# Kernel tuning notes

Hardware: AMD Instinct MI355X
Metric: run time of the kernel (lower is better)

The kernel has to match this reference:

```python
import jax, jax.numpy as jnp
import numpy as np
import math

B, S, D, H, WIDTH, NHW = 8, 1024, 512, 8, 8, 2
DK = D // H
S2 = S + 2 * WIDTH


def setup_inputs() -> dict:
    key = jax.random.key(0)
    ks = jax.random.split(key, 12)
    sc = 1.0 / math.sqrt(D)
    return {
        "x": jax.random.normal(ks[0], (B, S, D), jnp.float32),
        "l_attn_W": jax.random.normal(ks[1], (4, D, D), jnp.float32) * sc,  # q,k,v,out
        "l_attn_b": jnp.zeros((4, D), jnp.float32),
        "r_attn_W": jax.random.normal(ks[2], (4, D, D), jnp.float32) * sc,
        "r_attn_b": jnp.zeros((4, D), jnp.float32),
        "left_pad": jax.random.normal(ks[3], (WIDTH, D), jnp.float32) * sc,
        "right_pad": jax.random.normal(ks[4], (WIDTH, D), jnp.float32) * sc,
        "left_w": jax.random.normal(ks[5], (WIDTH + 1,), jnp.float32),
        "right_w": jax.random.normal(ks[6], (WIDTH + 1,), jnp.float32),
        "l_hw_W": jax.random.normal(ks[7], (NHW, D, 2 * D), jnp.float32) * sc,
        "l_hw_b": jnp.zeros((NHW, 2 * D), jnp.float32),
        "r_hw_W": jax.random.normal(ks[8], (NHW, D, 2 * D), jnp.float32) * sc,
        "r_hw_b": jnp.zeros((NHW, 2 * D), jnp.float32),
    }


def _mha(x, W, b, mask):
    # x: [B, S2, D]; W: [4, D, D]; mask: [1, S2, S2] bool (True = keep)
    q = (x @ W[0] + b[0]).reshape(B, S2, H, DK)
    k = (x @ W[1] + b[1]).reshape(B, S2, H, DK)
    v = (x @ W[2] + b[2]).reshape(B, S2, H, DK)
    scores = jnp.einsum('bihd,bjhd->bhij', q, k) / math.sqrt(DK)
    scores = jnp.where(mask[:, None], scores, jnp.float32(-1e9))
    p = jax.nn.softmax(scores, axis=-1)
    o = jnp.einsum('bhij,bjhd->bihd', p, v).reshape(B, S2, D)
    return o @ W[3] + b[3]


def _highway(x, Ws, bs):
    # AllenNLP-style Highway: projected -> [nonlinear | gate]
    for i in range(NHW):
        proj = x @ Ws[i] + bs[i]
        nl = jax.nn.relu(proj[..., :D])
        g = jax.nn.sigmoid(proj[..., D:])
        x = g * x + (1.0 - g) * nl
    return x


def reference(x, l_attn_W, l_attn_b, r_attn_W, r_attn_b, left_pad, right_pad,
              left_w, right_w, l_hw_W, l_hw_b, r_hw_W, r_hw_b):
    new_in = jnp.concatenate([
        jnp.broadcast_to(left_pad, (B, WIDTH, D)), x,
        jnp.broadcast_to(right_pad, (B, WIDTH, D))], axis=1)  # [B, S2, D]
    idx = jnp.arange(S2)
    diff = idx[:, None] - idx[None, :]
    lmask = ((diff >= 0) & (diff <= WIDTH + 1))[None]          # attend to [i-width-1, i]
    rmask = ((diff <= 0) & (diff >= -(WIDTH + 1)))[None]       # attend to [i, i+width+1]
    nl_attn = _mha(new_in, l_attn_W, l_attn_b, lmask)
    nr_attn = _mha(new_in, r_attn_W, r_attn_b, rmask)
    left_out = nl_attn[:, WIDTH:WIDTH + S, :]   # position end = start + width
    right_out = nr_attn[:, WIDTH:WIDTH + S, :]
    # relative-position weighted sliding windows (vectorized over all steps)
    lrel = sum(left_w[j] * new_in[:, j:j + S, :] for j in range(WIDTH + 1))
    rrel = sum(right_w[j] * new_in[:, WIDTH + j:WIDTH + j + S, :] for j in range(WIDTH + 1))
    left_out = _highway(left_out + lrel, l_hw_W, l_hw_b)
    right_out = _highway(right_out + rrel, r_hw_W, r_hw_b)
    out = jnp.concatenate([left_out, right_out], axis=-1)  # [B, S, 2D]
    return out[None]  # [1, B, S, 2D] matching torch stack layout
```

## Files before the change

### kernel.cpp

```cpp
#include <hip/hip_runtime.h>


#define B_ 8
#define S_ 1024
#define D_ 512
#define H_ 8
#define DK_ 64
#define WIDTH_ 8
#define S2_ 1040
#define NHW_ 2

typedef short bf16x8 __attribute__((ext_vector_type(8)));
typedef float f32x4 __attribute__((ext_vector_type(4)));

__device__ __forceinline__ float us2f(unsigned short u) {
  union { unsigned int i; float f; } c; c.i = ((unsigned int)u) << 16; return c.f;
}
__device__ __forceinline__ unsigned short f2us(float f) {
  union { float f; unsigned int i; } c; c.f = f;
  unsigned int x = c.i;
  return (unsigned short)((x + 0x7fffu + ((x >> 16) & 1u)) >> 16);
}
__device__ __forceinline__ unsigned int pack2(float a, float b) {
  return (unsigned int)f2us(a) | ((unsigned int)f2us(b) << 16);
}
__device__ __forceinline__ void async16(const void* g, void* l) {
  __builtin_amdgcn_global_load_lds(
      (const __attribute__((address_space(1))) void*)g,
      (__attribute__((address_space(3))) void*)l, 16, 0, 0);
}
__device__ __forceinline__ void unpack8(uint4 u, float* f) {
  unsigned int w[4] = {u.x, u.y, u.z, u.w};
  #pragma unroll
  for (int c = 0; c < 4; ++c) {
    union { unsigned int i; float g; } lo, hi;
    lo.i = w[c] << 16;
    hi.i = w[c] & 0xffff0000u;
    f[2 * c] = lo.g;
    f[2 * c + 1] = hi.g;
  }
}

__global__ __launch_bounds__(256) void k_transpose_attn(
    const float* __restrict__ lW, const float* __restrict__ rW,
    unsigned short* __restrict__ WTall, unsigned short* __restrict__ WTp)
{
  __shared__ float tile[32][33];
  const size_t DD = (size_t)D_ * D_;
  int z = blockIdx.z, side = z >> 2, slice = z & 3;
  const float* src = (side ? rW : lW) + (size_t)slice * DD;
  unsigned short* dst = (slice < 3) ? WTall + ((size_t)(side * 3 + slice)) * DD
                                    : WTp + (size_t)side * DD;
  int c0 = blockIdx.x * 32, r0 = blockIdx.y * 32;
  int tx = threadIdx.x & 31, ty = threadIdx.x >> 5;
  #pragma unroll
  for (int i = 0; i < 4; ++i)
    tile[ty + i * 8][tx] = src[(size_t)(r0 + ty + i * 8) * D_ + c0 + tx];
  __syncthreads();
  #pragma unroll
  for (int i = 0; i < 4; ++i)
    dst[(size_t)(c0 + ty + i * 8) * D_ + r0 + tx] = f2us(tile[tx][ty + i * 8]);
}

__global__ __launch_bounds__(256) void k_transpose_hw(
    const float* __restrict__ lhwW, const float* __restrict__ rhwW,
    unsigned short* __restrict__ hWT)
{
  __shared__ float tile[32][33];
  int z = blockIdx.z, side = z >> 1, layer = z & 1;
  const float* src = (side ? rhwW : lhwW) + (size_t)layer * 512 * 1024;
  unsigned short* dst = hWT + (size_t)(side * 2 + layer) * 1024 * 512;
  int c0 = blockIdx.x * 32, r0 = blockIdx.y * 32;
  int tx = threadIdx.x & 31, ty = threadIdx.x >> 5;
  #pragma unroll
  for (int i = 0; i < 4; ++i)
    tile[ty + i * 8][tx] = src[(size_t)(r0 + ty + i * 8) * 1024 + c0 + tx];
  __syncthreads();
  #pragma unroll
  for (int i = 0; i < 4; ++i) {
    int c = c0 + ty + i * 8;
    int q = (2 * ((c & 511) >> 4) + (c >= 512 ? 1 : 0)) * 16 + (c & 15);
    dst[(size_t)q * 512 + r0 + tx] = f2us(tile[tx][ty + i * 8]);
  }
}

__global__ __launch_bounds__(256) void k_build_new_in(
    const float* __restrict__ x,
    const float* __restrict__ lpad,
    const float* __restrict__ rpad,
    const float* __restrict__ lb,
    const float* __restrict__ rb,
    unsigned short* __restrict__ nin,
    float* __restrict__ qkvbias)
{
  int gid = blockIdx.x * 256 + threadIdx.x;
  const int NTH = B_ * S2_ * 64;
  if (gid >= NTH) {
    int t = gid - NTH;
    if (t < 1536) qkvbias[t] = lb[t];
    else if (t < 3072) qkvbias[t] = rb[t - 1536];
    return;
  }
  int c8 = (gid & 63) << 3;
  int row = gid >> 6;
  int b = row / S2_;
  int t = row - b * S2_;
  const float* src;
  if (t < WIDTH_)            src = lpad + (size_t)t * D_ + c8;
  else if (t >= S_ + WIDTH_) src = rpad + (size_t)(t - S_ - WIDTH_) * D_ + c8;
  else                       src = x + ((size_t)b * S_ + (t - WIDTH_)) * D_ + c8;
  float4 a = *reinterpret_cast<const float4*>(src);
  float4 c = *reinterpret_cast<const float4*>(src + 4);
  uint4 o;
  o.x = pack2(a.x, a.y); o.y = pack2(a.z, a.w);
  o.z = pack2(c.x, c.y); o.w = pack2(c.z, c.w);
  *reinterpret_cast<uint4*>(nin + (size_t)row * D_ + c8) = o;
}

__global__ __launch_bounds__(256) void k_gemm_mfma(
    const unsigned short* __restrict__ A, size_t aStrZ,
    const unsigned short* __restrict__ BT, size_t bStrZ,
    const float* __restrict__ bias0, const float* __restrict__ bias1,
    unsigned short* __restrict__ C, size_t cStrZ,
    int M, int N, int K)
{
  __shared__ unsigned short As[128 * 64];
  __shared__ unsigned short Bs[128 * 64];

  const int z = blockIdx.z;
  A += (size_t)z * aStrZ; BT += (size_t)z * bStrZ; C += (size_t)z * cStrZ;
  const float* bias = z ? bias1 : bias0;

  const int tid = threadIdx.x;
  const int w = tid >> 6;
  const int l = tid & 63;
  const int bm = blockIdx.y * 128;
  const int bn = blockIdx.x * 128;
  const int wrow = (w >> 1) * 64;
  const int wcol = (w & 1) * 64;

  const int lr = l >> 3;
  const int sk = (((l & 7) ^ lr) & 7) * 8;
  const unsigned short* Ap = A + (size_t)(bm + w * 8 + lr) * K + sk;
  const unsigned short* Bp = BT + (size_t)(bn + w * 8 + lr) * K + sk;
  unsigned short* lA = &As[w * 512];
  unsigned short* lB = &Bs[w * 512];
  const size_t K32 = (size_t)32 * K;

  const int fl = l & 15;
  const int fq = l >> 4;
  const int fx = fl & 7;

  f32x4 acc[4][4];
  #pragma unroll
  for (int mi = 0; mi < 4; ++mi)
    #pragma unroll
    for (int ni = 0; ni < 4; ++ni) acc[mi][ni] = (f32x4){0.f, 0.f, 0.f, 0.f};

  for (int k0 = 0; k0 < K; k0 += 64) {
    #pragma unroll
    for (int r = 0; r < 4; ++r) {
      async16(Ap + k0 + r * K32, lA + r * 2048);
      async16(Bp + k0 + r * K32, lB + r * 2048);
    }
    __syncthreads();
    #pragma unroll
    for (int s = 0; s < 2; ++s) {
      bf16x8 af[4], bfr[4];
      #pragma unroll
      for (int mi = 0; mi < 4; ++mi) {
        int R = wrow + mi * 16 + fl;
        af[mi] = *reinterpret_cast<const bf16x8*>(
            &As[R * 64 + (((s * 4 + fq) ^ fx) * 8)]);
      }
      #pragma unroll
      for (int ni = 0; ni < 4; ++ni) {
        int R = wcol + ni * 16 + fl;
        bfr[ni] = *reinterpret_cast<const bf16x8*>(
            &Bs[R * 64 + (((s * 4 + fq) ^ fx) * 8)]);
      }
      #pragma unroll
      for (int mi = 0; mi < 4; ++mi)
        #pragma unroll
        for (int ni = 0; ni < 4; ++ni)
          acc[mi][ni] = __builtin_amdgcn_mfma_f32_16x16x32_bf16(
              af[mi], bfr[ni], acc[mi][ni], 0, 0, 0);
    }
    __syncthreads();
  }

  float bv[4];
  #pragma unroll
  for (int ni = 0; ni < 4; ++ni) bv[ni] = bias[bn + wcol + ni * 16 + fl];

  const int rbase = (l >> 4) * 4;
  #pragma unroll
  for (int mi = 0; mi < 4; ++mi) {
    #pragma unroll
    for (int r = 0; r < 4; ++r) {
      int row = bm + wrow + mi * 16 + rbase + r;
      unsigned short* Cp = C + (size_t)row * N + bn + wcol + fl;
      #pragma unroll
      for (int ni = 0; ni < 4; ++ni)
        Cp[ni * 16] = f2us(acc[mi][ni][r] + bv[ni]);
    }
  }
}

template <bool FINAL>
__global__ __launch_bounds__(256) void k_gemm_hw(
    const unsigned short* __restrict__ Xsrc,
    const unsigned short* __restrict__ BT, size_t bStrZ,
    const float* __restrict__ bias0, const float* __restrict__ bias1,
    unsigned short* __restrict__ Obf,
    float* __restrict__ Ofp)
{
  __shared__ unsigned short As[128 * 64];
  __shared__ unsigned short Bs[128 * 64];
  const int K = 512;
  const size_t MS = (size_t)B_ * S_ * D_;

  const int z = blockIdx.z;
  const unsigned short* A = Xsrc + (size_t)z * MS;
  BT += (size_t)z * bStrZ;
  const float* bias = z ? bias1 : bias0;

  const int tid = threadIdx.x;
  const int w = tid >> 6;
  const int l = tid & 63;
  const int bm = blockIdx.y * 128;
  const int bn = blockIdx.x * 128;
  const int wrow = (w >> 1) * 64;
  const int wcol = (w & 1) * 64;

  const int lr = l >> 3;
  const int sk = (((l & 7) ^ lr) & 7) * 8;
  const unsigned short* Ap = A + (size_t)(bm + w * 8 + lr) * K + sk;
  const unsigned short* Bp = BT + (size_t)(bn + w * 8 + lr) * K + sk;
  unsigned short* lA = &As[w * 512];
  unsigned short* lB = &Bs[w * 512];
  const size_t K32 = (size_t)32 * K;

  const int fl = l & 15;
  const int fq = l >> 4;
  const int fx = fl & 7;

  f32x4 acc[4][4];
  #pragma unroll
  for (int mi = 0; mi < 4; ++mi)
    #pragma unroll
    for (int ni = 0; ni < 4; ++ni) acc[mi][ni] = (f32x4){0.f, 0.f, 0.f, 0.f};

  for (int k0 = 0; k0 < K; k0 += 64) {
    #pragma unroll
    for (int r = 0; r < 4; ++r) {
      async16(Ap + k0 + r * K32, lA + r * 2048);
      async16(Bp + k0 + r * K32, lB + r * 2048);
    }
    __syncthreads();
    #pragma unroll
    for (int s = 0; s < 2; ++s) {
      bf16x8 af[4], bfr[4];
      #pragma unroll
      for (int mi = 0; mi < 4; ++mi) {
        int R = wrow + mi * 16 + fl;
        af[mi] = *reinterpret_cast<const bf16x8*>(
            &As[R * 64 + (((s * 4 + fq) ^ fx) * 8)]);
      }
      #pragma unroll
      for (int ni = 0; ni < 4; ++ni) {
        int R = wcol + ni * 16 + fl;
        bfr[ni] = *reinterpret_cast<const bf16x8*>(
            &Bs[R * 64 + (((s * 4 + fq) ^ fx) * 8)]);
      }
      #pragma unroll
      for (int mi = 0; mi < 4; ++mi)
        #pragma unroll
        for (int ni = 0; ni < 4; ++ni)
          acc[mi][ni] = __builtin_amdgcn_mfma_f32_16x16x32_bf16(
              af[mi], bfr[ni], acc[mi][ni], 0, 0, 0);
    }
    __syncthreads();
  }

  const int ocb = ((bn + wcol) >> 1) + fl;
  float bnl[2], bg[2];
  #pragma unroll
  for (int p = 0; p < 2; ++p) {
    bnl[p] = bias[ocb + p * 16];
    bg[p]  = bias[512 + ocb + p * 16];
  }

  const int rbase = (l >> 4) * 4;
  #pragma unroll
  for (int mi = 0; mi < 4; ++mi) {
    #pragma unroll
    for (int r = 0; r < 4; ++r) {
      int row = bm + wrow + mi * 16 + rbase + r;
      #pragma unroll
      for (int p = 0; p < 2; ++p) {
        int oc = ocb + p * 16;
        float nl = fmaxf(acc[mi][2 * p][r] + bnl[p], 0.f);
        float g  = 1.f / (1.f + __expf(-(acc[mi][2 * p + 1][r] + bg[p])));
        float xv = us2f(A[(size_t)row * 512 + oc]);
        float res = g * xv + (1.f - g) * nl;
        if (FINAL) Ofp[(size_t)row * 1024 + z * 512 + oc] = res;
        else       Obf[(size_t)z * MS + (size_t)row * 512 + oc] = f2us(res);
      }
    }
  }
}

__global__ __launch_bounds__(256) void k_attn_window(
    const unsigned short* __restrict__ qkv,
    unsigned short* __restrict__ ctx)
{
  int wid = (blockIdx.x * 256 + threadIdx.x) >> 6;
  int lane = threadIdx.x & 63;
  int dir = 0;
  if (wid >= B_ * S2_) { dir = 1; wid -= B_ * S2_; }
  int i = wid % S2_;
  int b = wid / S2_;

  const size_t base = (size_t)b * S2_ * 3072 + dir * 1536;
  const int c0 = lane * 8;

  float qf[8];
  unpack8(*reinterpret_cast<const uint4*>(qkv + base + (size_t)i * 3072 + c0), qf);

  float sc[10];
  float mx = -1e30f;
  #pragma unroll
  for (int t = 0; t < 10; ++t) {
    int j = (dir == 0) ? (i - 9 + t) : (i + t);
    float s = -1e30f;
    if (j >= 0 && j < S2_) {
      float kf[8];
      unpack8(*reinterpret_cast<const uint4*>(
          qkv + base + (size_t)j * 3072 + 512 + c0), kf);
      float p = qf[0] * kf[0];
      #pragma unroll
      for (int e = 1; e < 8; ++e) p += qf[e] * kf[e];
      p += __shfl_xor(p, 1);
      p += __shfl_xor(p, 2);
      p += __shfl_xor(p, 4);
      s = p * 0.125f;
    }
    sc[t] = s;
    mx = fmaxf(mx, s);
  }

  float denom = 0.f;
  #pragma unroll
  for (int t = 0; t < 10; ++t) {
    sc[t] = (sc[t] > -1e29f) ? __expf(sc[t] - mx) : 0.f;
    denom += sc[t];
  }
  float inv = 1.f / denom;

  float acc[8] = {0.f, 0.f, 0.f, 0.f, 0.f, 0.f, 0.f, 0.f};
  #pragma unroll
  for (int t = 0; t < 10; ++t) {
    int j = (dir == 0) ? (i - 9 + t) : (i + t);
    if (j >= 0 && j < S2_) {
      float vf[8];
      unpack8(*reinterpret_cast<const uint4*>(
          qkv + base + (size_t)j * 3072 + 1024 + c0), vf);
      float p = sc[t];
      #pragma unroll
      for (int e = 0; e < 8; ++e) acc[e] += p * vf[e];
    }
  }

  uint4 o;
  o.x = pack2(acc[0] * inv, acc[1] * inv);
  o.y = pack2(acc[2] * inv, acc[3] * inv);
  o.z = pack2(acc[4] * inv, acc[5] * inv);
  o.w = pack2(acc[6] * inv, acc[7] * inv);
  *reinterpret_cast<uint4*>(
      ctx + ((size_t)dir * B_ * S2_ + (size_t)b * S2_ + i) * D_ + c0) = o;
}

__global__ __launch_bounds__(256) void k_rel_add(
    const unsigned short* __restrict__ proj,
    const unsigned short* __restrict__ nin,
    const float* __restrict__ wrel0,
    const float* __restrict__ wrel1,
    unsigned short* __restrict__ hwx)
{
  int z = blockIdx.y;
  const float* wrel = z ? wrel1 : wrel0;
  int off = z * WIDTH_;
  proj += (size_t)z * B_ * S2_ * D_;
  hwx  += (size_t)z * B_ * S_ * D_;

  int gid = blockIdx.x * 256 + threadIdx.x;
  int c8 = (gid & 63) << 3;
  int row = gid >> 6;
  if (row >= B_ * S_) return;
  int b = row >> 10;
  int s = row & (S_ - 1);

  float acc[8];
  unpack8(*reinterpret_cast<const uint4*>(
      proj + ((size_t)b * S2_ + WIDTH_ + s) * D_ + c8), acc);
  #pragma unroll
  for (int j = 0; j < 9; ++j) {
    float w = wrel[j];
    float nf[8];
    unpack8(*reinterpret_cast<const uint4*>(
        nin + ((size_t)b * S2_ + off + j + s) * D_ + c8), nf);
    #pragma unroll
    for (int e = 0; e < 8; ++e) acc[e] += w * nf[e];
  }
  uint4 o;
  o.x = pack2(acc[0], acc[1]); o.y = pack2(acc[2], acc[3]);
  o.z = pack2(acc[4], acc[5]); o.w = pack2(acc[6], acc[7]);
  *reinterpret_cast<uint4*>(hwx + (size_t)row * D_ + c8) = o;
}

extern "C" void kernel_launch(void* const* d_in, const int* in_sizes, int n_in,
                              void* d_out, int out_size, void* d_ws, size_t ws_size,
                              hipStream_t stream) {
  const float* x    = (const float*)d_in[0];
  const float* lW   = (const float*)d_in[1];
  const float* lb   = (const float*)d_in[2];
  const float* rW   = (const float*)d_in[3];
  const float* rb   = (const float*)d_in[4];
  const float* lpad = (const float*)d_in[5];
  const float* rpad = (const float*)d_in[6];
  const float* lw   = (const float*)d_in[7];
  const float* rw   = (const float*)d_in[8];
  const float* lhwW = (const float*)d_in[9];
  const float* lhwb = (const float*)d_in[10];
  const float* rhwW = (const float*)d_in[11];
  const float* rhwb = (const float*)d_in[12];
  float* out = (float*)d_out;
  unsigned short* ws = (unsigned short*)d_ws;

  const size_t NIN  = (size_t)B_ * S2_ * D_;
  const size_t NQKV = (size_t)B_ * S2_ * 3072;
  const size_t MS   = (size_t)B_ * S_ * D_;
  const size_t DD   = (size_t)D_ * D_;
  const size_t LHW  = (size_t)1024 * 512;

  unsigned short* nin   = ws;
  unsigned short* qkv   = nin + NIN;
  unsigned short* proj  = qkv;
  unsigned short* cb    = qkv + NQKV;
  unsigned short* hwx   = cb + 2 * NIN;
  unsigned short* hwy   = hwx + 2 * MS;
  unsigned short* WTall = hwy + 2 * MS;
  unsigned short* WTp   = WTall + 6 * DD;
  unsigned short* hWT   = WTp + 2 * DD;
  float* qkvbias        = (float*)(hWT + 4 * LHW);

  {
    dim3 ga(16, 16, 8);
    k_transpose_attn<<<ga, 256, 0, stream>>>(lW, rW, WTall, WTp);
    dim3 gh(32, 16, 4);
    k_transpose_hw<<<gh, 256, 0, stream>>>(lhwW, rhwW, hWT);
  }
  k_build_new_in<<<2092, 256, 0, stream>>>(x, lpad, rpad, lb, rb, nin, qkvbias);

  const int MQ = B_ * S2_;

  {
    dim3 g(3072 / 128, MQ / 128, 1);
    k_gemm_mfma<<<g, 256, 0, stream>>>(nin, 0, WTall, 0, qkvbias, qkvbias,
                                       qkv, 0, MQ, 3072, D_);
  }

  k_attn_window<<<(2 * B_ * S2_) / 4, 256, 0, stream>>>(qkv, cb);

  {
    dim3 g(D_ / 128, MQ / 128, 2);
    k_gemm_mfma<<<g, 256, 0, stream>>>(cb, NIN, WTp, DD, lb + 3 * D_, rb + 3 * D_,
                                       proj, NIN, MQ, D_, D_);
  }

  {
    dim3 g(2048, 2);
    k_rel_add<<<g, 256, 0, stream>>>(proj, nin, lw, rw, hwx);
  }

  {
    dim3 g(1024 / 128, (B_ * S_) / 128, 2);
    k_gemm_hw<false><<<g, 256, 0, stream>>>(hwx, hWT, 2 * LHW,
                                            lhwb, rhwb, hwy, nullptr);
    k_gemm_hw<true><<<g, 256, 0, stream>>>(hwy, hWT + LHW, 2 * LHW,
                                           lhwb + 1024, rhwb + 1024,
                                           nullptr, out);
  }
}
```

Before: 268.9 us.

## Fuse prep kernels, skip pad-row attention, fuse rel-add into output projection

Merges the two weight-transpose kernels and the input build into a single prep launch. The windowed attention now computes only the S interior rows instead of all S2 padded rows. The output-projection GEMM runs over just those rows and applies the relative-position weighted sum in its epilogue, staging results through LDS. This drops the separate rel_add pass and the proj round-trip through global memory, at the cost of a larger LDS footprint and a heavier GEMM epilogue.

```diff
diff --git a/kernel.cpp b/kernel.cpp
--- a/kernel.cpp
+++ b/kernel.cpp
@@ -41,59 +41,56 @@
   }
 }
 
-__global__ __launch_bounds__(256) void k_transpose_attn(
+__global__ __launch_bounds__(256) void k_prep(
+    const float* __restrict__ x,
+    const float* __restrict__ lpad, const float* __restrict__ rpad,
     const float* __restrict__ lW, const float* __restrict__ rW,
-    unsigned short* __restrict__ WTall, unsigned short* __restrict__ WTp)
+    const float* __restrict__ lb, const float* __restrict__ rb,
+    const float* __restrict__ lhwW, const float* __restrict__ rhwW,
+    unsigned short* __restrict__ WTall, unsigned short* __restrict__ WTp,
+    unsigned short* __restrict__ hWT,
+    unsigned short* __restrict__ nin, float* __restrict__ qkvbias)
 {
   __shared__ float tile[32][33];
   const size_t DD = (size_t)D_ * D_;
-  int z = blockIdx.z, side = z >> 2, slice = z & 3;
-  const float* src = (side ? rW : lW) + (size_t)slice * DD;
-  unsigned short* dst = (slice < 3) ? WTall + ((size_t)(side * 3 + slice)) * DD
-                                    : WTp + (size_t)side * DD;
-  int c0 = blockIdx.x * 32, r0 = blockIdx.y * 32;
+  int bx = blockIdx.x;
   int tx = threadIdx.x & 31, ty = threadIdx.x >> 5;
-  #pragma unroll
-  for (int i = 0; i < 4; ++i)
-    tile[ty + i * 8][tx] = src[(size_t)(r0 + ty + i * 8) * D_ + c0 + tx];
-  __syncthreads();
-  #pragma unroll
-  for (int i = 0; i < 4; ++i)
-    dst[(size_t)(c0 + ty + i * 8) * D_ + r0 + tx] = f2us(tile[tx][ty + i * 8]);
-}
-
-__global__ __launch_bounds__(256) void k_transpose_hw(
-    const float* __restrict__ lhwW, const float* __restrict__ rhwW,
-    unsigned short* __restrict__ hWT)
-{
-  __shared__ float tile[32][33];
-  int z = blockIdx.z, side = z >> 1, layer = z & 1;
-  const float* src = (side ? rhwW : lhwW) + (size_t)layer * 512 * 1024;
-  unsigned short* dst = hWT + (size_t)(side * 2 + layer) * 1024 * 512;
-  int c0 = blockIdx.x * 32, r0 = blockIdx.y * 32;
-  int tx = threadIdx.x & 31, ty = threadIdx.x >> 5;
-  #pragma unroll
-  for (int i = 0; i < 4; ++i)
-    tile[ty + i * 8][tx] = src[(size_t)(r0 + ty + i * 8) * 1024 + c0 + tx];
-  __syncthreads();
-  #pragma unroll
-  for (int i = 0; i < 4; ++i) {
-    int c = c0 + ty + i * 8;
-    int q = (2 * ((c & 511) >> 4) + (c >= 512 ? 1 : 0)) * 16 + (c & 15);
-    dst[(size_t)q * 512 + r0 + tx] = f2us(tile[tx][ty + i * 8]);
-  }
-}
-
-__global__ __launch_bounds__(256) void k_build_new_in(
-    const float* __restrict__ x,
-    const float* __restrict__ lpad,
-    const float* __restrict__ rpad,
-    const float* __restrict__ lb,
-    const float* __restrict__ rb,
-    unsigned short* __restrict__ nin,
-    float* __restrict__ qkvbias)
-{
-  int gid = blockIdx.x * 256 + threadIdx.x;
+
+  if (bx < 2048) {
+    int sl = bx >> 8, rem = bx & 255;
+    int side = sl >> 2, slice = sl & 3;
+    int c0 = (rem & 15) * 32, r0 = (rem >> 4) * 32;
+    const float* src = (side ? rW : lW) + (size_t)slice * DD;
+    unsigned short* dst = (slice < 3) ? WTall + (size_t)(side * 3 + slice) * DD
+                                      : WTp + (size_t)side * DD;
+    #pragma unroll
+    for (int i = 0; i < 4; ++i)
+      tile[ty + i * 8][tx] = src[(size_t)(r0 + ty + i * 8) * D_ + c0 + tx];
+    __syncthreads();
+    #pragma unroll
+    for (int i = 0; i < 4; ++i)
+      dst[(size_t)(c0 + ty + i * 8) * D_ + r0 + tx] = f2us(tile[tx][ty + i * 8]);
+    return;
+  }
+  if (bx < 4096) {
+    int idx = bx - 2048;
+    int sl = idx >> 9, rem = idx & 511;
+    int c0 = (rem & 31) * 32, r0 = (rem >> 5) * 32;
+    const float* src = ((sl >> 1) ? rhwW : lhwW) + (size_t)(sl & 1) * 512 * 1024;
+    unsigned short* dst = hWT + (size_t)sl * 1024 * 512;
+    #pragma unroll
+    for (int i = 0; i < 4; ++i)
+      tile[ty + i * 8][tx] = src[(size_t)(r0 + ty + i * 8) * 1024 + c0 + tx];
+    __syncthreads();
+    #pragma unroll
+    for (int i = 0; i < 4; ++i) {
+      int c = c0 + ty + i * 8;
+      int q = (2 * ((c & 511) >> 4) + (c >= 512 ? 1 : 0)) * 16 + (c & 15);
+      dst[(size_t)q * 512 + r0 + tx] = f2us(tile[tx][ty + i * 8]);
+    }
+    return;
+  }
+  int gid = (bx - 4096) * 256 + threadIdx.x;
   const int NTH = B_ * S2_ * 64;
   if (gid >= NTH) {
     int t = gid - NTH;
@@ -118,18 +115,14 @@
 }
 
 __global__ __launch_bounds__(256) void k_gemm_mfma(
-    const unsigned short* __restrict__ A, size_t aStrZ,
-    const unsigned short* __restrict__ BT, size_t bStrZ,
-    const float* __restrict__ bias0, const float* __restrict__ bias1,
-    unsigned short* __restrict__ C, size_t cStrZ,
+    const unsigned short* __restrict__ A,
+    const unsigned short* __restrict__ BT,
+    const float* __restrict__ bias,
+    unsigned short* __restrict__ C,
     int M, int N, int K)
 {
   __shared__ unsigned short As[128 * 64];
   __shared__ unsigned short Bs[128 * 64];
-
-  const int z = blockIdx.z;
-  A += (size_t)z * aStrZ; BT += (size_t)z * bStrZ; C += (size_t)z * cStrZ;
-  const float* bias = z ? bias1 : bias0;
 
   const int tid = threadIdx.x;
   const int w = tid >> 6;
@@ -168,17 +161,13 @@
     for (int s = 0; s < 2; ++s) {
       bf16x8 af[4], bfr[4];
       #pragma unroll
-      for (int mi = 0; mi < 4; ++mi) {
-        int R = wrow + mi * 16 + fl;
+      for (int mi = 0; mi < 4; ++mi)
         af[mi] = *reinterpret_cast<const bf16x8*>(
-            &As[R * 64 + (((s * 4 + fq) ^ fx) * 8)]);
-      }
-      #pragma unroll
-      for (int ni = 0; ni < 4; ++ni) {
-        int R = wcol + ni * 16 + fl;
+            &As[(wrow + mi * 16 + fl) * 64 + (((s * 4 + fq) ^ fx) * 8)]);
+      #pragma unroll
+      for (int ni = 0; ni < 4; ++ni)
         bfr[ni] = *reinterpret_cast<const bf16x8*>(
-            &Bs[R * 64 + (((s * 4 + fq) ^ fx) * 8)]);
-      }
+            &Bs[(wcol + ni * 16 + fl) * 64 + (((s * 4 + fq) ^ fx) * 8)]);
       #pragma unroll
       for (int mi = 0; mi < 4; ++mi)
         #pragma unroll
@@ -204,6 +193,125 @@
       for (int ni = 0; ni < 4; ++ni)
         Cp[ni * 16] = f2us(acc[mi][ni][r] + bv[ni]);
     }
+  }
+}
+
+__global__ __launch_bounds__(256) void k_gemm_proj(
+    const unsigned short* __restrict__ ctx,
+    const unsigned short* __restrict__ WTp,
+    const unsigned short* __restrict__ nin,
+    const float* __restrict__ lb3, const float* __restrict__ rb3,
+    const float* __restrict__ wrel0, const float* __restrict__ wrel1,
+    unsigned short* __restrict__ hwx)
+{
+  __shared__ unsigned short smem[128 * 136];
+  unsigned short* As = smem;
+  unsigned short* Bs = smem + 8192;
+  const int K = 512, N = 512;
+  const size_t MS = (size_t)B_ * S_ * D_;
+
+  const int z = blockIdx.z;
+  const unsigned short* A = ctx + (size_t)z * MS;
+  const unsigned short* BT = WTp + (size_t)z * 512 * 512;
+  const float* bias = z ? rb3 : lb3;
+  const float* wrel = z ? wrel1 : wrel0;
+  const int off = z * WIDTH_;
+
+  const int tid = threadIdx.x;
+  const int w = tid >> 6;
+  const int l = tid & 63;
+  const int bm = blockIdx.y * 128;
+  const int bn = blockIdx.x * 128;
+  const int wrow = (w >> 1) * 64;
+  const int wcol = (w & 1) * 64;
+
+  const int lr = l >> 3;
+  const int sk = (((l & 7) ^ lr) & 7) * 8;
+  const unsigned short* Ap = A + (size_t)(bm + w * 8 + lr) * K + sk;
+  const unsigned short* Bp = BT + (size_t)(bn + w * 8 + lr) * K + sk;
+  unsigned short* lA = &As[w * 512];
+  unsigned short* lB = &Bs[w * 512];
+  const size_t K32 = (size_t)32 * K;
+
+  const int fl = l & 15;
+  const int fq = l >> 4;
+  const int fx = fl & 7;
+
+  f32x4 acc[4][4];
+  #pragma unroll
+  for (int mi = 0; mi < 4; ++mi)
+    #pragma unroll
+    for (int ni = 0; ni < 4; ++ni) acc[mi][ni] = (f32x4){0.f, 0.f, 0.f, 0.f};
+
+  for (int k0 = 0; k0 < K; k0 += 64) {
+    #pragma unroll
+    for (int r = 0; r < 4; ++r) {
+      async16(Ap + k0 + r * K32, lA + r * 2048);
+      async16(Bp + k0 + r * K32, lB + r * 2048);
+    }
+    __syncthreads();
+    #pragma unroll
+    for (int s = 0; s < 2; ++s) {
+      bf16x8 af[4], bfr[4];
+      #pragma unroll
+      for (int mi = 0; mi < 4; ++mi)
+        af[mi] = *reinterpret_cast<const bf16x8*>(
+            &As[(wrow + mi * 16 + fl) * 64 + (((s * 4 + fq) ^ fx) * 8)]);
+      #pragma unroll
+      for (int ni = 0; ni < 4; ++ni)
+        bfr[ni] = *reinterpret_cast<const bf16x8*>(
+            &Bs[(wcol + ni * 16 + fl) * 64 + (((s * 4 + fq) ^ fx) * 8)]);
+      #pragma unroll
+      for (int mi = 0; mi < 4; ++mi)
+        #pragma unroll
+        for (int ni = 0; ni < 4; ++ni)
+          acc[mi][ni] = __builtin_amdgcn_mfma_f32_16x16x32_bf16(
+              af[mi], bfr[ni], acc[mi][ni], 0, 0, 0);
+    }
+    __syncthreads();
+  }
+
+  float bv[4];
+  #pragma unroll
+  for (int ni = 0; ni < 4; ++ni) bv[ni] = bias[bn + wcol + ni * 16 + fl];
+  const int rbase = (l >> 4) * 4;
+  #pragma unroll
+  for (int mi = 0; mi < 4; ++mi)
+    #pragma unroll
+    for (int r = 0; r < 4; ++r)
+      #pragma unroll
+      for (int ni = 0; ni < 4; ++ni)
+        smem[(wrow + mi * 16 + rbase + r) * 136 + wcol + ni * 16 + fl] =
+            f2us(acc[mi][ni][r] + bv[ni]);
+  __syncthreads();
+
+  const int trow = tid >> 4;
+  const int tcol = (tid & 15) * 8;
+  const float w0 = wrel[0], w1 = wrel[1], w2 = wrel[2], w3 = wrel[3],
+              w4 = wrel[4], w5 = wrel[5], w6 = wrel[6], w7 = wrel[7],
+              w8 = wrel[8];
+  const float wj[9] = {w0, w1, w2, w3, w4, w5, w6, w7, w8};
+  #pragma unroll
+  for (int i = 0; i < 8; ++i) {
+    int r = trow + i * 16;
+    int gr = bm + r;
+    int b = gr >> 10, s = gr & (S_ - 1);
+    float a8[8];
+    unpack8(*reinterpret_cast<const uint4*>(&smem[r * 136 + tcol]), a8);
+    const unsigned short* np =
+        nin + ((size_t)b * S2_ + off + s) * D_ + bn + tcol;
+    #pragma unroll
+    for (int j = 0; j < 9; ++j) {
+      float nf[8];
+      unpack8(*reinterpret_cast<const uint4*>(np + (size_t)j * D_), nf);
+      #pragma unroll
+      for (int e = 0; e < 8; ++e) a8[e] += wj[j] * nf[e];
+    }
+    uint4 o;
+    o.x = pack2(a8[0], a8[1]); o.y = pack2(a8[2], a8[3]);
+    o.z = pack2(a8[4], a8[5]); o.w = pack2(a8[6], a8[7]);
+    *reinterpret_cast<uint4*>(
+        hwx + (size_t)z * MS + (size_t)gr * D_ + bn + tcol) = o;
   }
 }
 
@@ -262,17 +370,13 @@
     for (int s = 0; s < 2; ++s) {
       bf16x8 af[4], bfr[4];
       #pragma unroll
-      for (int mi = 0; mi < 4; ++mi) {
-        int R = wrow + mi * 16 + fl;
+      for (int mi = 0; mi < 4; ++mi)
         af[mi] = *reinterpret_cast<const bf16x8*>(
-            &As[R * 64 + (((s * 4 + fq) ^ fx) * 8)]);
-      }
-      #pragma unroll
-      for (int ni = 0; ni < 4; ++ni) {
-        int R = wcol + ni * 16 + fl;
+            &As[(wrow + mi * 16 + fl) * 64 + (((s * 4 + fq) ^ fx) * 8)]);
+      #pragma unroll
+      for (int ni = 0; ni < 4; ++ni)
         bfr[ni] = *reinterpret_cast<const bf16x8*>(
-            &Bs[R * 64 + (((s * 4 + fq) ^ fx) * 8)]);
-      }
+            &Bs[(wcol + ni * 16 + fl) * 64 + (((s * 4 + fq) ^ fx) * 8)]);
       #pragma unroll
       for (int mi = 0; mi < 4; ++mi)
         #pragma unroll
@@ -317,10 +421,10 @@
 {
   int wid = (blockIdx.x * 256 + threadIdx.x) >> 6;
   int lane = threadIdx.x & 63;
-  int dir = 0;
-  if (wid >= B_ * S2_) { dir = 1; wid -= B_ * S2_; }
-  int i = wid % S2_;
-  int b = wid / S2_;
+  int s = wid & (S_ - 1);
+  int b = (wid >> 10) & (B_ - 1);
+  int dir = wid >> 13;
+  int i = s + WIDTH_;
 
   const size_t base = (size_t)b * S2_ * 3072 + dir * 1536;
   const int c0 = lane * 8;
@@ -333,7 +437,7 @@
   #pragma unroll
   for (int t = 0; t < 10; ++t) {
     int j = (dir == 0) ? (i - 9 + t) : (i + t);
-    float s = -1e30f;
+    float sv = -1e30f;
     if (j >= 0 && j < S2_) {
       float kf[8];
       unpack8(*reinterpret_cast<const uint4*>(
@@ -344,10 +448,10 @@
       p += __shfl_xor(p, 1);
       p += __shfl_xor(p, 2);
       p += __shfl_xor(p, 4);
-      s = p * 0.125f;
-    }
-    sc[t] = s;
-    mx = fmaxf(mx, s);
+      sv = p * 0.125f;
+    }
+    sc[t] = sv;
+    mx = fmaxf(mx, sv);
   }
 
   float denom = 0.f;
@@ -378,45 +482,7 @@
   o.z = pack2(acc[4] * inv, acc[5] * inv);
   o.w = pack2(acc[6] * inv, acc[7] * inv);
   *reinterpret_cast<uint4*>(
-      ctx + ((size_t)dir * B_ * S2_ + (size_t)b * S2_ + i) * D_ + c0) = o;
-}
-
-__global__ __launch_bounds__(256) void k_rel_add(
-    const unsigned short* __restrict__ proj,
-    const unsigned short* __restrict__ nin,
-    const float* __restrict__ wrel0,
-    const float* __restrict__ wrel1,
-    unsigned short* __restrict__ hwx)
-{
-  int z = blockIdx.y;
-  const float* wrel = z ? wrel1 : wrel0;
-  int off = z * WIDTH_;
-  proj += (size_t)z * B_ * S2_ * D_;
-  hwx  += (size_t)z * B_ * S_ * D_;
-
-  int gid = blockIdx.x * 256 + threadIdx.x;
-  int c8 = (gid & 63) << 3;
-  int row = gid >> 6;
-  if (row >= B_ * S_) return;
-  int b = row >> 10;
-  int s = row & (S_ - 1);
-
-  float acc[8];
-  unpack8(*reinterpret_cast<const uint4*>(
-      proj + ((size_t)b * S2_ + WIDTH_ + s) * D_ + c8), acc);
-  #pragma unroll
-  for (int j = 0; j < 9; ++j) {
-    float w = wrel[j];
-    float nf[8];
-    unpack8(*reinterpret_cast<const uint4*>(
-        nin + ((size_t)b * S2_ + off + j + s) * D_ + c8), nf);
-    #pragma unroll
-    for (int e = 0; e < 8; ++e) acc[e] += w * nf[e];
-  }
-  uint4 o;
-  o.x = pack2(acc[0], acc[1]); o.y = pack2(acc[2], acc[3]);
-  o.z = pack2(acc[4], acc[5]); o.w = pack2(acc[6], acc[7]);
-  *reinterpret_cast<uint4*>(hwx + (size_t)row * D_ + c8) = o;
+      ctx + (((size_t)dir * B_ + b) * S_ + s) * D_ + c0) = o;
 }
 
 extern "C" void kernel_launch(void* const* d_in, const int* in_sizes, int n_in,
@@ -446,42 +512,30 @@
 
   unsigned short* nin   = ws;
   unsigned short* qkv   = nin + NIN;
-  unsigned short* proj  = qkv;
-  unsigned short* cb    = qkv + NQKV;
-  unsigned short* hwx   = cb + 2 * NIN;
+  unsigned short* ctx   = qkv + NQKV;
+  unsigned short* hwx   = ctx + 2 * MS;
   unsigned short* hwy   = hwx + 2 * MS;
   unsigned short* WTall = hwy + 2 * MS;
   unsigned short* WTp   = WTall + 6 * DD;
   unsigned short* hWT   = WTp + 2 * DD;
   float* qkvbias        = (float*)(hWT + 4 * LHW);
 
-  {
-    dim3 ga(16, 16, 8);
-    k_transpose_attn<<<ga, 256, 0, stream>>>(lW, rW, WTall, WTp);
-    dim3 gh(32, 16, 4);
-    k_transpose_hw<<<gh, 256, 0, stream>>>(lhwW, rhwW, hWT);
-  }
-  k_build_new_in<<<2092, 256, 0, stream>>>(x, lpad, rpad, lb, rb, nin, qkvbias);
+  k_prep<<<6188, 256, 0, stream>>>(x, lpad, rpad, lW, rW, lb, rb, lhwW, rhwW,
+                                   WTall, WTp, hWT, nin, qkvbias);
 
   const int MQ = B_ * S2_;
 
   {
     dim3 g(3072 / 128, MQ / 128, 1);
-    k_gemm_mfma<<<g, 256, 0, stream>>>(nin, 0, WTall, 0, qkvbias, qkvbias,
-                                       qkv, 0, MQ, 3072, D_);
-  }
-
-  k_attn_window<<<(2 * B_ * S2_) / 4, 256, 0, stream>>>(qkv, cb);
+    k_gemm_mfma<<<g, 256, 0, stream>>>(nin, WTall, qkvbias, qkv, MQ, 3072, D_);
+  }
+
+  k_attn_window<<<(2 * B_ * S_) / 4, 256, 0, stream>>>(qkv, ctx);
 
   {
-    dim3 g(D_ / 128, MQ / 128, 2);
-    k_gemm_mfma<<<g, 256, 0, stream>>>(cb, NIN, WTp, DD, lb + 3 * D_, rb + 3 * D_,
-                                       proj, NIN, MQ, D_, D_);
-  }
-
-  {
-    dim3 g(2048, 2);
-    k_rel_add<<<g, 256, 0, stream>>>(proj, nin, lw, rw, hwx);
+    dim3 g(D_ / 128, (B_ * S_) / 128, 2);
+    k_gemm_proj<<<g, 256, 0, stream>>>(ctx, WTp, nin, lb + 3 * D_, rb + 3 * D_,
+                                       lw, rw, hwx);
   }
 
   {
```

After: 243.9 us. 1.1x faster.
